# Performance work log

Hardware: AMD Instinct MI355X
Metric: run time of the kernel (lower is better)

Reference implementation:

```python
import jax, jax.numpy as jnp
import numpy as np

EMBED = 1024
HEADS = 16

def setup_inputs() -> dict:
    key = jax.random.key(0)
    ks = jax.random.split(key, 6)
    N, S = 1, 4096
    half = EMBED // 2
    x = jax.random.normal(ks[0], (N, S, EMBED), dtype=jnp.float32)
    Wq = jax.random.normal(ks[1], (half, half), dtype=jnp.float32) * 0.02
    Wk = jax.random.normal(ks[2], (half, half), dtype=jnp.float32) * 0.02
    Wv = jax.random.normal(ks[3], (half, half), dtype=jnp.float32) * 0.02
    Wo = jax.random.normal(ks[4], (EMBED, half), dtype=jnp.float32) * 0.02
    bo = jnp.zeros((EMBED,), dtype=jnp.float32)
    return {"x": x, "Wq": Wq, "Wk": Wk, "Wv": Wv, "Wo": Wo, "bo": bo}

def reference(x, Wq, Wk, Wv, Wo, bo):
    N, S, E = x.shape
    H = HEADS
    Dh = (E // 2) // H                 # per-head dim of the half-width projections (32)
    scale = float(E // H) ** 0.5       # original scales by head_dim = embed/heads = 64
    left = x[..., : E // 2]            # only the left chunk feeds attention in the source
    # torch Linear: y = x @ W.T (no bias)
    q = (left @ Wq.T).reshape(N, S, H, Dh)
    k = (left @ Wk.T).reshape(N, S, H, Dh)
    v = (left @ Wv.T).reshape(N, S, H, Dh)
    energy = jnp.einsum('nqhd,nkhd->nqkh', q, k)          # [N,S,S,H] full score tensor
    att = jax.nn.softmax(energy / scale, axis=2)          # softmax over key axis
    out = jnp.einsum('nqkh,nkhd->nqhd', att, v)           # [N,S,H,Dh]
    out = out.reshape(N, S, E // 2)
    return out @ Wo.T + bo                                # fc_out: half -> embed
```

## Files before the change

### kernel.cpp

```cpp
#include <hip/hip_runtime.h>
#include <stdint.h>


#define SEQ    4096
#define DMODEL 1024
#define DHALF  512
#define NH     16
#define DH     32

typedef __attribute__((ext_vector_type(4))) float facc4;
typedef __attribute__((ext_vector_type(8))) short bfrag8;

#define MFMA_BF16(a, b, c) __builtin_amdgcn_mfma_f32_16x16x32_bf16((a), (b), (c), 0, 0, 0)

static __device__ __forceinline__ uint16_t f2b(float x) {
    uint32_t u = __float_as_uint(x);
    return (uint16_t)((u + 0x7FFFu + ((u >> 16) & 1u)) >> 16);
}
static __device__ __forceinline__ float b2f(uint16_t b) {
    return __uint_as_float(((uint32_t)b) << 16);
}

static __device__ __forceinline__ bfrag8 cvt8perm(float4 a, float4 b) {
    uint32_t u0 = __float_as_uint(a.x) + 0x8000u, u1 = __float_as_uint(a.y) + 0x8000u;
    uint32_t u2 = __float_as_uint(a.z) + 0x8000u, u3 = __float_as_uint(a.w) + 0x8000u;
    uint32_t u4 = __float_as_uint(b.x) + 0x8000u, u5 = __float_as_uint(b.y) + 0x8000u;
    uint32_t u6 = __float_as_uint(b.z) + 0x8000u, u7 = __float_as_uint(b.w) + 0x8000u;
    union { uint32_t w[4]; bfrag8 r; } u;
    u.w[0] = __builtin_amdgcn_perm(u1, u0, 0x07060302u);
    u.w[1] = __builtin_amdgcn_perm(u3, u2, 0x07060302u);
    u.w[2] = __builtin_amdgcn_perm(u5, u4, 0x07060302u);
    u.w[3] = __builtin_amdgcn_perm(u7, u6, 0x07060302u);
    return u.r;
}

__global__ __launch_bounds__(256) void convert_w(
    const float* __restrict__ Wq, const float* __restrict__ Wk,
    const float* __restrict__ Wv, const float* __restrict__ Wo,
    uint16_t* __restrict__ q, uint16_t* __restrict__ k,
    uint16_t* __restrict__ v, uint16_t* __restrict__ o)
{
    int zz = blockIdx.x;
    const float* src; uint16_t* dst; size_t off;
    if      (zz < 128) { src = Wq; dst = q; off = (size_t)zz * 2048; }
    else if (zz < 256) { src = Wk; dst = k; off = (size_t)(zz - 128) * 2048; }
    else if (zz < 384) { src = Wv; dst = v; off = (size_t)(zz - 256) * 2048; }
    else               { src = Wo; dst = o; off = (size_t)(zz - 384) * 2048; }
    size_t i = off + (size_t)threadIdx.x * 8;
    float4 a = *(const float4*)&src[i];
    float4 b = *(const float4*)&src[i + 4];
    *(bfrag8*)&dst[i] = cvt8perm(a, b);
}

template <int AF32>
__device__ __forceinline__ void gemm128T(
    const void* __restrict__ A, int lda,
    const uint16_t* __restrict__ B, int ldb,
    void* __restrict__ C, int ldc, int cF32,
    const float* __restrict__ bias, float scale,
    int Kd, int m0, int n0)
{
    __shared__ __align__(16) uint16_t As[2][128 * 40];
    __shared__ __align__(16) uint16_t Bs[2][128 * 40];

    const int tid  = threadIdx.x;
    const int lane = tid & 63;
    const int wv   = tid >> 6;
    const int lo   = lane & 15;
    const int quad = lane >> 4;
    const int srow = tid >> 2;
    const int skq  = (tid & 3) * 8;
    const int rb   = (wv >> 1) * 64;
    const int cb   = (wv & 1) * 64;

    const facc4 ZACC = {0.f, 0.f, 0.f, 0.f};
    facc4 acc[4][4];
#pragma unroll
    for (int i = 0; i < 4; ++i)
#pragma unroll
        for (int j = 0; j < 4; ++j) acc[i][j] = ZACC;

    const float*    fA0 = AF32 ? &((const float*)A)[(size_t)(m0 + srow) * lda + skq] : nullptr;
    const float*    fA1 = AF32 ? &((const float*)A)[(size_t)(m0 + srow + 64) * lda + skq] : nullptr;
    const uint16_t* hA0 = AF32 ? nullptr : &((const uint16_t*)A)[(size_t)(m0 + srow) * lda + skq];
    const uint16_t* hA1 = AF32 ? nullptr : &((const uint16_t*)A)[(size_t)(m0 + srow + 64) * lda + skq];
    const uint16_t* pB0 = &B[(size_t)(n0 + srow) * ldb + skq];
    const uint16_t* pB1 = &B[(size_t)(n0 + srow + 64) * ldb + skq];

    bfrag8 ra0, ra1;
    float4 f0a, f0b, f1a, f1b;
    if (AF32) {
        f0a = *(const float4*)fA0; f0b = *(const float4*)(fA0 + 4);
        f1a = *(const float4*)fA1; f1b = *(const float4*)(fA1 + 4);
    } else {
        ra0 = *(const bfrag8*)hA0;
        ra1 = *(const bfrag8*)hA1;
    }
    bfrag8 rb0 = *(const bfrag8*)pB0;
    bfrag8 rb1 = *(const bfrag8*)pB1;

    if (AF32) {
        *(bfrag8*)&As[0][srow * 40 + skq]        = cvt8perm(f0a, f0b);
        *(bfrag8*)&As[0][(srow + 64) * 40 + skq] = cvt8perm(f1a, f1b);
    } else {
        *(bfrag8*)&As[0][srow * 40 + skq]        = ra0;
        *(bfrag8*)&As[0][(srow + 64) * 40 + skq] = ra1;
    }
    *(bfrag8*)&Bs[0][srow * 40 + skq]        = rb0;
    *(bfrag8*)&Bs[0][(srow + 64) * 40 + skq] = rb1;
    __syncthreads();

    int p = 0;
    for (int kt = 0; kt < Kd; kt += 32) {
        const bool more = (kt + 32 < Kd);
        if (more) {
            if (AF32) {
                f0a = *(const float4*)(fA0 + kt + 32); f0b = *(const float4*)(fA0 + kt + 36);
                f1a = *(const float4*)(fA1 + kt + 32); f1b = *(const float4*)(fA1 + kt + 36);
            } else {
                ra0 = *(const bfrag8*)(hA0 + kt + 32);
                ra1 = *(const bfrag8*)(hA1 + kt + 32);
            }
            rb0 = *(const bfrag8*)(pB0 + kt + 32);
            rb1 = *(const bfrag8*)(pB1 + kt + 32);
        }

        bfrag8 af[4], bf[4];
#pragma unroll
        for (int i = 0; i < 4; ++i) {
            af[i] = *(const bfrag8*)&As[p][(rb + i * 16 + lo) * 40 + quad * 8];
            bf[i] = *(const bfrag8*)&Bs[p][(cb + i * 16 + lo) * 40 + quad * 8];
        }
#pragma unroll
        for (int i = 0; i < 4; ++i)
#pragma unroll
            for (int j = 0; j < 4; ++j)
                acc[i][j] = MFMA_BF16(af[i], bf[j], acc[i][j]);

        if (more) {
            if (AF32) {
                *(bfrag8*)&As[1 - p][srow * 40 + skq]        = cvt8perm(f0a, f0b);
                *(bfrag8*)&As[1 - p][(srow + 64) * 40 + skq] = cvt8perm(f1a, f1b);
            } else {
                *(bfrag8*)&As[1 - p][srow * 40 + skq]        = ra0;
                *(bfrag8*)&As[1 - p][(srow + 64) * 40 + skq] = ra1;
            }
            *(bfrag8*)&Bs[1 - p][srow * 40 + skq]        = rb0;
            *(bfrag8*)&Bs[1 - p][(srow + 64) * 40 + skq] = rb1;
            __syncthreads();
            p ^= 1;
        }
    }

#pragma unroll
    for (int j = 0; j < 4; ++j) {
        int col  = n0 + cb + j * 16 + lo;
        float bv = bias ? bias[col] : 0.f;
#pragma unroll
        for (int i = 0; i < 4; ++i) {
#pragma unroll
            for (int r = 0; r < 4; ++r) {
                int row = m0 + rb + i * 16 + quad * 4 + r;
                float v = acc[i][j][r] * scale + bv;
                if (cF32) ((float*)C)[(size_t)row * ldc + col] = v;
                else      ((uint16_t*)C)[(size_t)row * ldc + col] = f2b(v);
            }
        }
    }
}

#define SC_Q (0.125f * 1.4426950408889634f)

__global__ __launch_bounds__(256, 2) void qkv_kernel(
    const float* __restrict__ x,
    const uint16_t* __restrict__ Wqb, const uint16_t* __restrict__ Wkb,
    const uint16_t* __restrict__ Wvb,
    uint16_t* __restrict__ Q, uint16_t* __restrict__ K, uint16_t* __restrict__ V)
{
    const int z = blockIdx.z;
    const uint16_t* W = (z == 0) ? Wqb : (z == 1) ? Wkb : Wvb;
    uint16_t* Out     = (z == 0) ? Q   : (z == 1) ? K   : V;
    float scale       = (z == 0) ? SC_Q : 1.0f;
    gemm128T<1>(x, DMODEL, W, DHALF, Out, DHALF, 0, nullptr, scale, DHALF,
                blockIdx.y * 128, blockIdx.x * 128);
}

__global__ __launch_bounds__(256, 2) void outproj_kernel(
    const uint16_t* __restrict__ O, const uint16_t* __restrict__ Wob,
    const float* __restrict__ bo, float* __restrict__ Y)
{
    gemm128T<0>(O, DHALF, Wob, DHALF, Y, DMODEL, 1, bo, 1.0f, DHALF,
                blockIdx.y * 128, blockIdx.x * 128);
}

__global__ __launch_bounds__(256) void attn_kernel(
    const uint16_t* __restrict__ Q, const uint16_t* __restrict__ Kb,
    const uint16_t* __restrict__ Vb, uint16_t* __restrict__ Op,
    float* __restrict__ lbuf, int kspan)
{
    __shared__ __align__(16) uint16_t Ks[2][64 * 40];
    __shared__ __align__(16) uint16_t Vt[2][32 * 64];

    const int tid  = threadIdx.x;
    const int lane = tid & 63;
    const int wv   = tid >> 6;
    const int lo   = lane & 15;
    const int quad = lane >> 4;
    const int h    = blockIdx.y;
    const int q0   = blockIdx.x * 128;
    const int sp   = blockIdx.z;
    const int srow = tid >> 2;
    const int skq  = (tid & 3) * 8;

    const facc4 ZACC = {0.f, 0.f, 0.f, 0.f};

    bfrag8 qf[2];
    qf[0] = *(const bfrag8*)&Q[(size_t)(q0 + wv * 32 + lo) * DHALF + h * DH + quad * 8];
    qf[1] = *(const bfrag8*)&Q[(size_t)(q0 + wv * 32 + 16 + lo) * DHALF + h * DH + quad * 8];

    bfrag8 ones;
#pragma unroll
    for (int j = 0; j < 8; ++j) ones[j] = (short)0x3F80;

    int vt_w[8];
    {
        int pb = ((srow >> 5) << 2) | ((srow >> 2) & 3);
        int pw = (((srow >> 4) & 1) << 2) | (srow & 3);
#pragma unroll
        for (int j = 0; j < 8; ++j) {
            int d  = skq + j;
            int Rd = ((d & 7) + 2 * (d >> 3)) & 7;
            vt_w[j] = d * 64 + (((pb + Rd) & 7) << 3) + pw;
        }
    }
    int vt_r[2][2];
#pragma unroll
    for (int dt = 0; dt < 2; ++dt) {
        int d  = dt * 16 + lo;
        int Rd = ((d & 7) + 2 * (d >> 3)) & 7;
#pragma unroll
        for (int c = 0; c < 2; ++c)
            vt_r[c][dt] = d * 64 + ((((c * 4 + quad) + Rd) & 7) << 3);
    }
    const int ks_r = lo * 40 + quad * 8;

    const uint16_t* kp = &Kb[(size_t)(sp * kspan + srow) * DHALF + h * DH + skq];
    const uint16_t* vp = &Vb[(size_t)(sp * kspan + srow) * DHALF + h * DH + skq];

    facc4 oacc[2][2], oaccL[2];
    oacc[0][0] = ZACC; oacc[0][1] = ZACC;
    oacc[1][0] = ZACC; oacc[1][1] = ZACC;
    oaccL[0] = ZACC; oaccL[1] = ZACC;

    float4 kreg = *(const float4*)kp;
    float4 vreg = *(const float4*)vp;
    kp += 64 * DHALF;
    vp += 64 * DHALF;

#define STAGE(BUF) do {                                                       \
        *(float4*)&Ks[BUF][srow * 40 + skq] = kreg;                           \
        const uint16_t* vsp = (const uint16_t*)&vreg;                         \
        _Pragma("unroll")                                                     \
        for (int j = 0; j < 8; ++j) Vt[BUF][vt_w[j]] = vsp[j];                \
    } while (0)

#define TILE(BUF) do {                                                        \
        uint2 w0[4], w1[4];                                                   \
        _Pragma("unroll")                                                     \
        for (int t4 = 0; t4 < 4; ++t4) {                                      \
            bfrag8 kf = *(const bfrag8*)&Ks[BUF][t4 * 640 + ks_r];            \
            facc4 s0 = MFMA_BF16(kf, qf[0], ZACC);                            \
            facc4 s1 = MFMA_BF16(kf, qf[1], ZACC);                            \
            uint32_t a0 = __float_as_uint(__builtin_amdgcn_exp2f(s0[0])) + 0x8000u; \
            uint32_t a1 = __float_as_uint(__builtin_amdgcn_exp2f(s0[1])) + 0x8000u; \
            uint32_t a2 = __float_as_uint(__builtin_amdgcn_exp2f(s0[2])) + 0x8000u; \
            uint32_t a3 = __float_as_uint(__builtin_amdgcn_exp2f(s0[3])) + 0x8000u; \
            w0[t4].x = __builtin_amdgcn_perm(a1, a0, 0x07060302u);            \
            w0[t4].y = __builtin_amdgcn_perm(a3, a2, 0x07060302u);            \
            uint32_t b0 = __float_as_uint(__builtin_amdgcn_exp2f(s1[0])) + 0x8000u; \
            uint32_t b1 = __float_as_uint(__builtin_amdgcn_exp2f(s1[1])) + 0x8000u; \
            uint32_t b2 = __float_as_uint(__builtin_amdgcn_exp2f(s1[2])) + 0x8000u; \
            uint32_t b3 = __float_as_uint(__builtin_amdgcn_exp2f(s1[3])) + 0x8000u; \
            w1[t4].x = __builtin_amdgcn_perm(b1, b0, 0x07060302u);            \
            w1[t4].y = __builtin_amdgcn_perm(b3, b2, 0x07060302u);            \
        }                                                                     \
        union PU { uint2 u2[2]; bfrag8 f; } pu;                               \
        bfrag8 pf0[2], pf1[2];                                                \
        pu.u2[0] = w0[0]; pu.u2[1] = w0[1]; pf0[0] = pu.f;                    \
        pu.u2[0] = w0[2]; pu.u2[1] = w0[3]; pf0[1] = pu.f;                    \
        pu.u2[0] = w1[0]; pu.u2[1] = w1[1]; pf1[0] = pu.f;                    \
        pu.u2[0] = w1[2]; pu.u2[1] = w1[3]; pf1[1] = pu.f;                    \
        _Pragma("unroll")                                                     \
        for (int c = 0; c < 2; ++c) {                                         \
            _Pragma("unroll")                                                 \
            for (int dt = 0; dt < 2; ++dt) {                                  \
                bfrag8 vf = *(const bfrag8*)&Vt[BUF][vt_r[c][dt]];            \
                oacc[0][dt] = MFMA_BF16(pf0[c], vf, oacc[0][dt]);             \
                oacc[1][dt] = MFMA_BF16(pf1[c], vf, oacc[1][dt]);             \
            }                                                                 \
            oaccL[0] = MFMA_BF16(pf0[c], ones, oaccL[0]);                     \
            oaccL[1] = MFMA_BF16(pf1[c], ones, oaccL[1]);                     \
        }                                                                     \
    } while (0)

    STAGE(0);
    __syncthreads();

    const int nt = kspan >> 6;
    for (int t = 0; t < nt; t += 2) {
        kreg = *(const float4*)kp;
        vreg = *(const float4*)vp;
        kp += 64 * DHALF; vp += 64 * DHALF;
        TILE(0);
        STAGE(1);
        __syncthreads();

        const bool more = (t + 2 < nt);
        if (more) {
            kreg = *(const float4*)kp;
            vreg = *(const float4*)vp;
            kp += 64 * DHALF; vp += 64 * DHALF;
        }
        TILE(1);
        if (more) {
            STAGE(0);
            __syncthreads();
        }
    }
#undef STAGE
#undef TILE

    if (lo == 0) {
#pragma unroll
        for (int g = 0; g < 2; ++g)
#pragma unroll
            for (int r = 0; r < 4; ++r)
                lbuf[((size_t)sp * NH + h) * SEQ + q0 + wv * 32 + g * 16 + quad * 4 + r] =
                    oaccL[g][r];
    }

    uint16_t* Od = Op + (size_t)sp * SEQ * DHALF;
#pragma unroll
    for (int g = 0; g < 2; ++g) {
#pragma unroll
        for (int r = 0; r < 4; ++r) {
            int row = q0 + wv * 32 + g * 16 + quad * 4 + r;
            Od[(size_t)row * DHALF + h * DH + lo]      = f2b(oacc[g][0][r]);
            Od[(size_t)row * DHALF + h * DH + 16 + lo] = f2b(oacc[g][1][r]);
        }
    }
}

__global__ __launch_bounds__(256) void combine_kernel(
    const uint16_t* __restrict__ Op, const float* __restrict__ lbuf,
    uint16_t* __restrict__ O, int ns)
{
    int t   = blockIdx.x * 256 + threadIdx.x;
    int row = t >> 6;
    int cb  = (t & 63) << 3;
    int h   = cb >> 5;
    float l = 0.f;
    float acc[8] = {0.f, 0.f, 0.f, 0.f, 0.f, 0.f, 0.f, 0.f};
    for (int sp = 0; sp < ns; ++sp) {
        l += lbuf[((size_t)sp * NH + h) * SEQ + row];
        bfrag8 a = *(const bfrag8*)&Op[(size_t)sp * SEQ * DHALF + (size_t)row * DHALF + cb];
#pragma unroll
        for (int j = 0; j < 8; ++j) acc[j] += b2f((uint16_t)a[j]);
    }
    float inv = 1.0f / l;
    bfrag8 o;
#pragma unroll
    for (int j = 0; j < 8; ++j) o[j] = (short)f2b(acc[j] * inv);
    *(bfrag8*)&O[(size_t)row * DHALF + cb] = o;
}

extern "C" void kernel_launch(void* const* d_in, const int* in_sizes, int n_in,
                              void* d_out, int out_size, void* d_ws, size_t ws_size,
                              hipStream_t stream)
{
    const float* x  = (const float*)d_in[0];
    const float* Wq = (const float*)d_in[1];
    const float* Wk = (const float*)d_in[2];
    const float* Wv = (const float*)d_in[3];
    const float* Wo = (const float*)d_in[4];
    const float* bo = (const float*)d_in[5];

    size_t fixed_e = 3 * (size_t)DHALF * DHALF + (size_t)DMODEL * DHALF
                   + 4 * (size_t)SEQ * DHALF;
    size_t need4 = (fixed_e + 4 * (size_t)SEQ * DHALF) * 2
                 + 4 * (size_t)NH * SEQ * 4;
    const int ns = (ws_size >= need4) ? 4 : 2;

    uint16_t* Wqb = (uint16_t*)d_ws;
    uint16_t* Wkb = Wqb + (size_t)DHALF * DHALF;
    uint16_t* Wvb = Wkb + (size_t)DHALF * DHALF;
    uint16_t* Wob = Wvb + (size_t)DHALF * DHALF;
    uint16_t* Q   = Wob + (size_t)DMODEL * DHALF;
    uint16_t* K   = Q + (size_t)SEQ * DHALF;
    uint16_t* V   = K + (size_t)SEQ * DHALF;
    uint16_t* O   = V + (size_t)SEQ * DHALF;
    uint16_t* Op  = O + (size_t)SEQ * DHALF;
    float*  lbuf  = (float*)(Op + (size_t)ns * SEQ * DHALF);

    convert_w<<<640, 256, 0, stream>>>(Wq, Wk, Wv, Wo, Wqb, Wkb, Wvb, Wob);
    qkv_kernel<<<dim3(DHALF / 128, SEQ / 128, 3), 256, 0, stream>>>(
        x, Wqb, Wkb, Wvb, Q, K, V);
    attn_kernel<<<dim3(SEQ / 128, NH, ns), 256, 0, stream>>>(Q, K, V, Op, lbuf, SEQ / ns);
    combine_kernel<<<1024, 256, 0, stream>>>(Op, lbuf, O, ns);
    outproj_kernel<<<dim3(DMODEL / 128, SEQ / 128), 256, 0, stream>>>(
        O, Wob, bo, (float*)d_out);
}
```

Baseline: 176.5 us.

## Software-pipeline attention QK/exp with PV across tiles; pre-convert x to bf16

```diff
diff --git a/kernel.cpp b/kernel.cpp
--- a/kernel.cpp
+++ b/kernel.cpp
@@ -37,10 +37,22 @@
 __global__ __launch_bounds__(256) void convert_w(
     const float* __restrict__ Wq, const float* __restrict__ Wk,
     const float* __restrict__ Wv, const float* __restrict__ Wo,
+    const float* __restrict__ x,
     uint16_t* __restrict__ q, uint16_t* __restrict__ k,
-    uint16_t* __restrict__ v, uint16_t* __restrict__ o)
+    uint16_t* __restrict__ v, uint16_t* __restrict__ o,
+    uint16_t* __restrict__ xb)
 {
     int zz = blockIdx.x;
+    if (zz >= 640) {
+        size_t g = (size_t)(zz - 640) * 2048 + (size_t)threadIdx.x * 8;
+        int row = (int)(g >> 9);
+        int col = (int)(g & 511);
+        const float* src = &x[(size_t)row * DMODEL + col];
+        float4 a = *(const float4*)src;
+        float4 b = *(const float4*)(src + 4);
+        *(bfrag8*)&xb[g] = cvt8perm(a, b);
+        return;
+    }
     const float* src; uint16_t* dst; size_t off;
     if      (zz < 128) { src = Wq; dst = q; off = (size_t)zz * 2048; }
     else if (zz < 256) { src = Wk; dst = k; off = (size_t)(zz - 128) * 2048; }
@@ -52,9 +64,8 @@
     *(bfrag8*)&dst[i] = cvt8perm(a, b);
 }
 
-template <int AF32>
-__device__ __forceinline__ void gemm128T(
-    const void* __restrict__ A, int lda,
+__device__ __forceinline__ void gemm128(
+    const uint16_t* __restrict__ A, int lda,
     const uint16_t* __restrict__ B, int ldb,
     void* __restrict__ C, int ldc, int cF32,
     const float* __restrict__ bias, float scale,
@@ -80,32 +91,18 @@
 #pragma unroll
         for (int j = 0; j < 4; ++j) acc[i][j] = ZACC;
 
-    const float*    fA0 = AF32 ? &((const float*)A)[(size_t)(m0 + srow) * lda + skq] : nullptr;
-    const float*    fA1 = AF32 ? &((const float*)A)[(size_t)(m0 + srow + 64) * lda + skq] : nullptr;
-    const uint16_t* hA0 = AF32 ? nullptr : &((const uint16_t*)A)[(size_t)(m0 + srow) * lda + skq];
-    const uint16_t* hA1 = AF32 ? nullptr : &((const uint16_t*)A)[(size_t)(m0 + srow + 64) * lda + skq];
+    const uint16_t* hA0 = &A[(size_t)(m0 + srow) * lda + skq];
+    const uint16_t* hA1 = &A[(size_t)(m0 + srow + 64) * lda + skq];
     const uint16_t* pB0 = &B[(size_t)(n0 + srow) * ldb + skq];
     const uint16_t* pB1 = &B[(size_t)(n0 + srow + 64) * ldb + skq];
 
-    bfrag8 ra0, ra1;
-    float4 f0a, f0b, f1a, f1b;
-    if (AF32) {
-        f0a = *(const float4*)fA0; f0b = *(const float4*)(fA0 + 4);
-        f1a = *(const float4*)fA1; f1b = *(const float4*)(fA1 + 4);
-    } else {
-        ra0 = *(const bfrag8*)hA0;
-        ra1 = *(const bfrag8*)hA1;
-    }
+    bfrag8 ra0 = *(const bfrag8*)hA0;
+    bfrag8 ra1 = *(const bfrag8*)hA1;
     bfrag8 rb0 = *(const bfrag8*)pB0;
     bfrag8 rb1 = *(const bfrag8*)pB1;
 
-    if (AF32) {
-        *(bfrag8*)&As[0][srow * 40 + skq]        = cvt8perm(f0a, f0b);
-        *(bfrag8*)&As[0][(srow + 64) * 40 + skq] = cvt8perm(f1a, f1b);
-    } else {
-        *(bfrag8*)&As[0][srow * 40 + skq]        = ra0;
-        *(bfrag8*)&As[0][(srow + 64) * 40 + skq] = ra1;
-    }
+    *(bfrag8*)&As[0][srow * 40 + skq]        = ra0;
+    *(bfrag8*)&As[0][(srow + 64) * 40 + skq] = ra1;
     *(bfrag8*)&Bs[0][srow * 40 + skq]        = rb0;
     *(bfrag8*)&Bs[0][(srow + 64) * 40 + skq] = rb1;
     __syncthreads();
@@ -114,13 +111,8 @@
     for (int kt = 0; kt < Kd; kt += 32) {
         const bool more = (kt + 32 < Kd);
         if (more) {
-            if (AF32) {
-                f0a = *(const float4*)(fA0 + kt + 32); f0b = *(const float4*)(fA0 + kt + 36);
-                f1a = *(const float4*)(fA1 + kt + 32); f1b = *(const float4*)(fA1 + kt + 36);
-            } else {
-                ra0 = *(const bfrag8*)(hA0 + kt + 32);
-                ra1 = *(const bfrag8*)(hA1 + kt + 32);
-            }
+            ra0 = *(const bfrag8*)(hA0 + kt + 32);
+            ra1 = *(const bfrag8*)(hA1 + kt + 32);
             rb0 = *(const bfrag8*)(pB0 + kt + 32);
             rb1 = *(const bfrag8*)(pB1 + kt + 32);
         }
@@ -138,13 +130,8 @@
                 acc[i][j] = MFMA_BF16(af[i], bf[j], acc[i][j]);
 
         if (more) {
-            if (AF32) {
-                *(bfrag8*)&As[1 - p][srow * 40 + skq]        = cvt8perm(f0a, f0b);
-                *(bfrag8*)&As[1 - p][(srow + 64) * 40 + skq] = cvt8perm(f1a, f1b);
-            } else {
-                *(bfrag8*)&As[1 - p][srow * 40 + skq]        = ra0;
-                *(bfrag8*)&As[1 - p][(srow + 64) * 40 + skq] = ra1;
-            }
+            *(bfrag8*)&As[1 - p][srow * 40 + skq]        = ra0;
+            *(bfrag8*)&As[1 - p][(srow + 64) * 40 + skq] = ra1;
             *(bfrag8*)&Bs[1 - p][srow * 40 + skq]        = rb0;
             *(bfrag8*)&Bs[1 - p][(srow + 64) * 40 + skq] = rb1;
             __syncthreads();
@@ -172,7 +159,7 @@
 #define SC_Q (0.125f * 1.4426950408889634f)
 
 __global__ __launch_bounds__(256, 2) void qkv_kernel(
-    const float* __restrict__ x,
+    const uint16_t* __restrict__ xb,
     const uint16_t* __restrict__ Wqb, const uint16_t* __restrict__ Wkb,
     const uint16_t* __restrict__ Wvb,
     uint16_t* __restrict__ Q, uint16_t* __restrict__ K, uint16_t* __restrict__ V)
@@ -181,16 +168,16 @@
     const uint16_t* W = (z == 0) ? Wqb : (z == 1) ? Wkb : Wvb;
     uint16_t* Out     = (z == 0) ? Q   : (z == 1) ? K   : V;
     float scale       = (z == 0) ? SC_Q : 1.0f;
-    gemm128T<1>(x, DMODEL, W, DHALF, Out, DHALF, 0, nullptr, scale, DHALF,
-                blockIdx.y * 128, blockIdx.x * 128);
+    gemm128(xb, DHALF, W, DHALF, Out, DHALF, 0, nullptr, scale, DHALF,
+            blockIdx.y * 128, blockIdx.x * 128);
 }
 
 __global__ __launch_bounds__(256, 2) void outproj_kernel(
     const uint16_t* __restrict__ O, const uint16_t* __restrict__ Wob,
     const float* __restrict__ bo, float* __restrict__ Y)
 {
-    gemm128T<0>(O, DHALF, Wob, DHALF, Y, DMODEL, 1, bo, 1.0f, DHALF,
-                blockIdx.y * 128, blockIdx.x * 128);
+    gemm128(O, DHALF, Wob, DHALF, Y, DMODEL, 1, bo, 1.0f, DHALF,
+            blockIdx.y * 128, blockIdx.x * 128);
 }
 
 __global__ __launch_bounds__(256) void attn_kernel(
@@ -199,7 +186,7 @@
     float* __restrict__ lbuf, int kspan)
 {
     __shared__ __align__(16) uint16_t Ks[2][64 * 40];
-    __shared__ __align__(16) uint16_t Vt[2][32 * 64];
+    __shared__ __align__(16) uint16_t Vt[4][32 * 64];
 
     const int tid  = threadIdx.x;
     const int lane = tid & 63;
@@ -252,23 +239,27 @@
     oacc[1][0] = ZACC; oacc[1][1] = ZACC;
     oaccL[0] = ZACC; oaccL[1] = ZACC;
 
-    float4 kreg = *(const float4*)kp;
-    float4 vreg = *(const float4*)vp;
-    kp += 64 * DHALF;
-    vp += 64 * DHALF;
-
-#define STAGE(BUF) do {                                                       \
-        *(float4*)&Ks[BUF][srow * 40 + skq] = kreg;                           \
+    float4 kreg, vreg;
+    bfrag8 pfA0[2], pfA1[2], pfB0[2], pfB1[2];
+
+#define LOADKV do {                                                           \
+        kreg = *(const float4*)kp;                                            \
+        vreg = *(const float4*)vp;                                            \
+        kp += 64 * DHALF; vp += 64 * DHALF;                                   \
+    } while (0)
+
+#define STAGE(KB, VB) do {                                                    \
+        *(float4*)&Ks[KB][srow * 40 + skq] = kreg;                            \
         const uint16_t* vsp = (const uint16_t*)&vreg;                         \
         _Pragma("unroll")                                                     \
-        for (int j = 0; j < 8; ++j) Vt[BUF][vt_w[j]] = vsp[j];                \
+        for (int j = 0; j < 8; ++j) Vt[VB][vt_w[j]] = vsp[j];                 \
     } while (0)
 
-#define TILE(BUF) do {                                                        \
+#define QKEXP(KB, PF0, PF1) do {                                              \
         uint2 w0[4], w1[4];                                                   \
         _Pragma("unroll")                                                     \
         for (int t4 = 0; t4 < 4; ++t4) {                                      \
-            bfrag8 kf = *(const bfrag8*)&Ks[BUF][t4 * 640 + ks_r];            \
+            bfrag8 kf = *(const bfrag8*)&Ks[KB][t4 * 640 + ks_r];             \
             facc4 s0 = MFMA_BF16(kf, qf[0], ZACC);                            \
             facc4 s1 = MFMA_BF16(kf, qf[1], ZACC);                            \
             uint32_t a0 = __float_as_uint(__builtin_amdgcn_exp2f(s0[0])) + 0x8000u; \
@@ -285,50 +276,73 @@
             w1[t4].y = __builtin_amdgcn_perm(b3, b2, 0x07060302u);            \
         }                                                                     \
         union PU { uint2 u2[2]; bfrag8 f; } pu;                               \
-        bfrag8 pf0[2], pf1[2];                                                \
-        pu.u2[0] = w0[0]; pu.u2[1] = w0[1]; pf0[0] = pu.f;                    \
-        pu.u2[0] = w0[2]; pu.u2[1] = w0[3]; pf0[1] = pu.f;                    \
-        pu.u2[0] = w1[0]; pu.u2[1] = w1[1]; pf1[0] = pu.f;                    \
-        pu.u2[0] = w1[2]; pu.u2[1] = w1[3]; pf1[1] = pu.f;                    \
+        pu.u2[0] = w0[0]; pu.u2[1] = w0[1]; PF0[0] = pu.f;                    \
+        pu.u2[0] = w0[2]; pu.u2[1] = w0[3]; PF0[1] = pu.f;                    \
+        pu.u2[0] = w1[0]; pu.u2[1] = w1[1]; PF1[0] = pu.f;                    \
+        pu.u2[0] = w1[2]; pu.u2[1] = w1[3]; PF1[1] = pu.f;                    \
+    } while (0)
+
+#define PV(VB, PF0, PF1) do {                                                 \
+        __builtin_amdgcn_s_setprio(1);                                        \
         _Pragma("unroll")                                                     \
         for (int c = 0; c < 2; ++c) {                                         \
             _Pragma("unroll")                                                 \
             for (int dt = 0; dt < 2; ++dt) {                                  \
-                bfrag8 vf = *(const bfrag8*)&Vt[BUF][vt_r[c][dt]];            \
-                oacc[0][dt] = MFMA_BF16(pf0[c], vf, oacc[0][dt]);             \
-                oacc[1][dt] = MFMA_BF16(pf1[c], vf, oacc[1][dt]);             \
+                bfrag8 vf = *(const bfrag8*)&Vt[VB][vt_r[c][dt]];             \
+                oacc[0][dt] = MFMA_BF16(PF0[c], vf, oacc[0][dt]);             \
+                oacc[1][dt] = MFMA_BF16(PF1[c], vf, oacc[1][dt]);             \
             }                                                                 \
-            oaccL[0] = MFMA_BF16(pf0[c], ones, oaccL[0]);                     \
-            oaccL[1] = MFMA_BF16(pf1[c], ones, oaccL[1]);                     \
+            oaccL[0] = MFMA_BF16(PF0[c], ones, oaccL[0]);                     \
+            oaccL[1] = MFMA_BF16(PF1[c], ones, oaccL[1]);                     \
         }                                                                     \
+        __builtin_amdgcn_s_setprio(0);                                        \
     } while (0)
 
-    STAGE(0);
+    const int nt = kspan >> 6;
+
+    LOADKV;
+    STAGE(0, 0);
     __syncthreads();
-
-    const int nt = kspan >> 6;
-    for (int t = 0; t < nt; t += 2) {
-        kreg = *(const float4*)kp;
-        vreg = *(const float4*)vp;
-        kp += 64 * DHALF; vp += 64 * DHALF;
-        TILE(0);
-        STAGE(1);
-        __syncthreads();
-
-        const bool more = (t + 2 < nt);
+    LOADKV;
+    QKEXP(0, pfA0, pfA1);
+    STAGE(1, 1); __syncthreads(); LOADKV;
+    QKEXP(1, pfB0, pfB1);
+    PV(0, pfA0, pfA1);
+    STAGE(0, 2); __syncthreads(); LOADKV;
+    QKEXP(0, pfA0, pfA1);
+    PV(1, pfB0, pfB1);
+    STAGE(1, 3); __syncthreads(); LOADKV;
+    QKEXP(1, pfB0, pfB1);
+    PV(2, pfA0, pfA1);
+    STAGE(0, 0); __syncthreads(); LOADKV;
+
+    for (int t = 4; t < nt; t += 4) {
+        QKEXP(0, pfA0, pfA1);
+        PV(3, pfB0, pfB1);
+        STAGE(1, 1); __syncthreads(); LOADKV;
+
+        QKEXP(1, pfB0, pfB1);
+        PV(0, pfA0, pfA1);
+        STAGE(0, 2); __syncthreads(); LOADKV;
+
+        QKEXP(0, pfA0, pfA1);
+        PV(1, pfB0, pfB1);
+        STAGE(1, 3); __syncthreads();
+        const bool more = (t + 4 < nt);
+        if (more) LOADKV;
+
+        QKEXP(1, pfB0, pfB1);
+        PV(2, pfA0, pfA1);
         if (more) {
-            kreg = *(const float4*)kp;
-            vreg = *(const float4*)vp;
-            kp += 64 * DHALF; vp += 64 * DHALF;
-        }
-        TILE(1);
-        if (more) {
-            STAGE(0);
-            __syncthreads();
-        }
-    }
+            STAGE(0, 0); __syncthreads(); LOADKV;
+        }
+    }
+    PV(3, pfB0, pfB1);
+
+#undef LOADKV
 #undef STAGE
-#undef TILE
+#undef QKEXP
+#undef PV
 
     if (lo == 0) {
 #pragma unroll
@@ -401,10 +415,11 @@
     uint16_t* O   = V + (size_t)SEQ * DHALF;
     uint16_t* Op  = O + (size_t)SEQ * DHALF;
     float*  lbuf  = (float*)(Op + (size_t)ns * SEQ * DHALF);
-
-    convert_w<<<640, 256, 0, stream>>>(Wq, Wk, Wv, Wo, Wqb, Wkb, Wvb, Wob);
+    uint16_t* xb  = O;
+
+    convert_w<<<1664, 256, 0, stream>>>(Wq, Wk, Wv, Wo, x, Wqb, Wkb, Wvb, Wob, xb);
     qkv_kernel<<<dim3(DHALF / 128, SEQ / 128, 3), 256, 0, stream>>>(
-        x, Wqb, Wkb, Wvb, Q, K, V);
+        xb, Wqb, Wkb, Wvb, Q, K, V);
     attn_kernel<<<dim3(SEQ / 128, NH, ns), 256, 0, stream>>>(Q, K, V, Op, lbuf, SEQ / ns);
     combine_kernel<<<1024, 256, 0, stream>>>(Op, lbuf, O, ns);
     outproj_kernel<<<dim3(DMODEL / 128, SEQ / 128), 256, 0, stream>>>(
```

Result: no change. 175.7 us (-0.5%).

## Pre-convert x left half to bf16 and remap attention block order

Applied to the files above, without the earlier changes.

```diff
diff --git a/kernel.cpp b/kernel.cpp
--- a/kernel.cpp
+++ b/kernel.cpp
@@ -37,10 +37,22 @@
 __global__ __launch_bounds__(256) void convert_w(
     const float* __restrict__ Wq, const float* __restrict__ Wk,
     const float* __restrict__ Wv, const float* __restrict__ Wo,
+    const float* __restrict__ x,
     uint16_t* __restrict__ q, uint16_t* __restrict__ k,
-    uint16_t* __restrict__ v, uint16_t* __restrict__ o)
+    uint16_t* __restrict__ v, uint16_t* __restrict__ o,
+    uint16_t* __restrict__ xb)
 {
     int zz = blockIdx.x;
+    if (zz >= 640) {
+        size_t g = (size_t)(zz - 640) * 2048 + (size_t)threadIdx.x * 8;
+        int row = (int)(g >> 9);
+        int col = (int)(g & 511);
+        const float* src = &x[(size_t)row * DMODEL + col];
+        float4 a = *(const float4*)src;
+        float4 b = *(const float4*)(src + 4);
+        *(bfrag8*)&xb[g] = cvt8perm(a, b);
+        return;
+    }
     const float* src; uint16_t* dst; size_t off;
     if      (zz < 128) { src = Wq; dst = q; off = (size_t)zz * 2048; }
     else if (zz < 256) { src = Wk; dst = k; off = (size_t)(zz - 128) * 2048; }
@@ -52,9 +64,8 @@
     *(bfrag8*)&dst[i] = cvt8perm(a, b);
 }
 
-template <int AF32>
-__device__ __forceinline__ void gemm128T(
-    const void* __restrict__ A, int lda,
+__device__ __forceinline__ void gemm128(
+    const uint16_t* __restrict__ A, int lda,
     const uint16_t* __restrict__ B, int ldb,
     void* __restrict__ C, int ldc, int cF32,
     const float* __restrict__ bias, float scale,
@@ -80,32 +91,18 @@
 #pragma unroll
         for (int j = 0; j < 4; ++j) acc[i][j] = ZACC;
 
-    const float*    fA0 = AF32 ? &((const float*)A)[(size_t)(m0 + srow) * lda + skq] : nullptr;
-    const float*    fA1 = AF32 ? &((const float*)A)[(size_t)(m0 + srow + 64) * lda + skq] : nullptr;
-    const uint16_t* hA0 = AF32 ? nullptr : &((const uint16_t*)A)[(size_t)(m0 + srow) * lda + skq];
-    const uint16_t* hA1 = AF32 ? nullptr : &((const uint16_t*)A)[(size_t)(m0 + srow + 64) * lda + skq];
+    const uint16_t* hA0 = &A[(size_t)(m0 + srow) * lda + skq];
+    const uint16_t* hA1 = &A[(size_t)(m0 + srow + 64) * lda + skq];
     const uint16_t* pB0 = &B[(size_t)(n0 + srow) * ldb + skq];
     const uint16_t* pB1 = &B[(size_t)(n0 + srow + 64) * ldb + skq];
 
-    bfrag8 ra0, ra1;
-    float4 f0a, f0b, f1a, f1b;
-    if (AF32) {
-        f0a = *(const float4*)fA0; f0b = *(const float4*)(fA0 + 4);
-        f1a = *(const float4*)fA1; f1b = *(const float4*)(fA1 + 4);
-    } else {
-        ra0 = *(const bfrag8*)hA0;
-        ra1 = *(const bfrag8*)hA1;
-    }
+    bfrag8 ra0 = *(const bfrag8*)hA0;
+    bfrag8 ra1 = *(const bfrag8*)hA1;
     bfrag8 rb0 = *(const bfrag8*)pB0;
     bfrag8 rb1 = *(const bfrag8*)pB1;
 
-    if (AF32) {
-        *(bfrag8*)&As[0][srow * 40 + skq]        = cvt8perm(f0a, f0b);
-        *(bfrag8*)&As[0][(srow + 64) * 40 + skq] = cvt8perm(f1a, f1b);
-    } else {
-        *(bfrag8*)&As[0][srow * 40 + skq]        = ra0;
-        *(bfrag8*)&As[0][(srow + 64) * 40 + skq] = ra1;
-    }
+    *(bfrag8*)&As[0][srow * 40 + skq]        = ra0;
+    *(bfrag8*)&As[0][(srow + 64) * 40 + skq] = ra1;
     *(bfrag8*)&Bs[0][srow * 40 + skq]        = rb0;
     *(bfrag8*)&Bs[0][(srow + 64) * 40 + skq] = rb1;
     __syncthreads();
@@ -114,13 +111,8 @@
     for (int kt = 0; kt < Kd; kt += 32) {
         const bool more = (kt + 32 < Kd);
         if (more) {
-            if (AF32) {
-                f0a = *(const float4*)(fA0 + kt + 32); f0b = *(const float4*)(fA0 + kt + 36);
-                f1a = *(const float4*)(fA1 + kt + 32); f1b = *(const float4*)(fA1 + kt + 36);
-            } else {
-                ra0 = *(const bfrag8*)(hA0 + kt + 32);
-                ra1 = *(const bfrag8*)(hA1 + kt + 32);
-            }
+            ra0 = *(const bfrag8*)(hA0 + kt + 32);
+            ra1 = *(const bfrag8*)(hA1 + kt + 32);
             rb0 = *(const bfrag8*)(pB0 + kt + 32);
             rb1 = *(const bfrag8*)(pB1 + kt + 32);
         }
@@ -138,13 +130,8 @@
                 acc[i][j] = MFMA_BF16(af[i], bf[j], acc[i][j]);
 
         if (more) {
-            if (AF32) {
-                *(bfrag8*)&As[1 - p][srow * 40 + skq]        = cvt8perm(f0a, f0b);
-                *(bfrag8*)&As[1 - p][(srow + 64) * 40 + skq] = cvt8perm(f1a, f1b);
-            } else {
-                *(bfrag8*)&As[1 - p][srow * 40 + skq]        = ra0;
-                *(bfrag8*)&As[1 - p][(srow + 64) * 40 + skq] = ra1;
-            }
+            *(bfrag8*)&As[1 - p][srow * 40 + skq]        = ra0;
+            *(bfrag8*)&As[1 - p][(srow + 64) * 40 + skq] = ra1;
             *(bfrag8*)&Bs[1 - p][srow * 40 + skq]        = rb0;
             *(bfrag8*)&Bs[1 - p][(srow + 64) * 40 + skq] = rb1;
             __syncthreads();
@@ -172,7 +159,7 @@
 #define SC_Q (0.125f * 1.4426950408889634f)
 
 __global__ __launch_bounds__(256, 2) void qkv_kernel(
-    const float* __restrict__ x,
+    const uint16_t* __restrict__ xb,
     const uint16_t* __restrict__ Wqb, const uint16_t* __restrict__ Wkb,
     const uint16_t* __restrict__ Wvb,
     uint16_t* __restrict__ Q, uint16_t* __restrict__ K, uint16_t* __restrict__ V)
@@ -181,16 +168,16 @@
     const uint16_t* W = (z == 0) ? Wqb : (z == 1) ? Wkb : Wvb;
     uint16_t* Out     = (z == 0) ? Q   : (z == 1) ? K   : V;
     float scale       = (z == 0) ? SC_Q : 1.0f;
-    gemm128T<1>(x, DMODEL, W, DHALF, Out, DHALF, 0, nullptr, scale, DHALF,
-                blockIdx.y * 128, blockIdx.x * 128);
+    gemm128(xb, DHALF, W, DHALF, Out, DHALF, 0, nullptr, scale, DHALF,
+            blockIdx.y * 128, blockIdx.x * 128);
 }
 
 __global__ __launch_bounds__(256, 2) void outproj_kernel(
     const uint16_t* __restrict__ O, const uint16_t* __restrict__ Wob,
     const float* __restrict__ bo, float* __restrict__ Y)
 {
-    gemm128T<0>(O, DHALF, Wob, DHALF, Y, DMODEL, 1, bo, 1.0f, DHALF,
-                blockIdx.y * 128, blockIdx.x * 128);
+    gemm128(O, DHALF, Wob, DHALF, Y, DMODEL, 1, bo, 1.0f, DHALF,
+            blockIdx.y * 128, blockIdx.x * 128);
 }
 
 __global__ __launch_bounds__(256) void attn_kernel(
@@ -206,9 +193,13 @@
     const int wv   = tid >> 6;
     const int lo   = lane & 15;
     const int quad = lane >> 4;
-    const int h    = blockIdx.y;
-    const int q0   = blockIdx.x * 128;
-    const int sp   = blockIdx.z;
+
+    const int f  = blockIdx.x + 32 * blockIdx.y + 512 * blockIdx.z;
+    const int pp = (f & 7) | ((f >> 8) << 3);
+    const int h  = pp & 15;
+    const int sp = pp >> 4;
+    const int q0 = ((f >> 3) & 31) * 128;
+
     const int srow = tid >> 2;
     const int skq  = (tid & 3) * 8;
 
@@ -401,10 +392,11 @@
     uint16_t* O   = V + (size_t)SEQ * DHALF;
     uint16_t* Op  = O + (size_t)SEQ * DHALF;
     float*  lbuf  = (float*)(Op + (size_t)ns * SEQ * DHALF);
-
-    convert_w<<<640, 256, 0, stream>>>(Wq, Wk, Wv, Wo, Wqb, Wkb, Wvb, Wob);
+    uint16_t* xb  = O;
+
+    convert_w<<<1664, 256, 0, stream>>>(Wq, Wk, Wv, Wo, x, Wqb, Wkb, Wvb, Wob, xb);
     qkv_kernel<<<dim3(DHALF / 128, SEQ / 128, 3), 256, 0, stream>>>(
-        x, Wqb, Wkb, Wvb, Q, K, V);
+        xb, Wqb, Wkb, Wvb, Q, K, V);
     attn_kernel<<<dim3(SEQ / 128, NH, ns), 256, 0, stream>>>(Q, K, V, Op, lbuf, SEQ / ns);
     combine_kernel<<<1024, 256, 0, stream>>>(Op, lbuf, O, ns);
     outproj_kernel<<<dim3(DMODEL / 128, SEQ / 128), 256, 0, stream>>>(
```

Result: faster. 169.2 us (-4.1%).
